# Kernel optimization log

Hardware: AMD Instinct MI355X
Metric: run time of the kernel (lower is better)

## Reference

```python
import jax, jax.numpy as jnp
import numpy as np
from jax import lax

# cell-group layout (order matters): sr_esoma, sr_edend, sr_pv, sr_sst, sr_vip, pfc_esoma, pfc_edend, pfc_pv, pfc_sst, pfc_vip
SIZES = [512, 1024, 128, 128, 128, 512, 1024, 128, 128, 128]
OFF = np.cumsum([0] + SIZES)
(SR_ES, SR_ED, SR_PV, SR_SST, SR_VIP,
 PFC_ES, PFC_ED, PFC_PV, PFC_SST, PFC_VIP) = [slice(int(OFF[i]), int(OFF[i + 1])) for i in range(10)]
N = int(OFF[-1])            # 3840 total neurons
N_BR = 2                    # dendritic branches per excitatory soma
N_IN, N_OUT = 128, 3
T, B = 100, 32
DT, TAU = 10.0, 50.0
DECAY = DT / TAU            # hp['dt']/hp['tau']
NOISE_STD = 0.01            # hp['network_noise']

# mGluR slow-integration coefficients on PFC E-dendrites: alpha_me = dt / logspace(100..5000), tiled over branches
_tau_me = np.tile(np.logspace(np.log10(100.0), np.log10(5000.0), SIZES[6] // N_BR), N_BR)
ALPHA_ME = jnp.asarray(DT / _tau_me, dtype=jnp.float32)   # [1024]

_dend = np.zeros(N, dtype=bool)
_dend[SR_ED] = True
_dend[PFC_ED] = True
DEND_VEC = jnp.asarray(_dend)


def _build_mask():
    """Dale's-law connectivity mask: +1 excitatory rows, -1 inhibitory rows,
    dend->own-region soma blocked (handled by dend2soma), zero diagonal."""
    m = np.ones((N, N), dtype=np.float32)
    for inh in (SR_PV, SR_SST, SR_VIP, PFC_PV, PFC_SST, PFC_VIP):
        m[inh, :] = -1.0
    m[SR_ED, SR_ES] = 0.0
    m[PFC_ED, PFC_ES] = 0.0
    np.fill_diagonal(m, 0.0)
    return m


def setup_inputs() -> dict:
    key = jax.random.key(0)
    ks = jax.random.split(key, 5)
    return {
        "x": jax.random.normal(ks[0], (T, B, N_IN), jnp.float32),
        "noise": jax.random.normal(ks[1], (T, B, N), jnp.float32),
        "w_rec": jax.random.normal(ks[2], (N, N), jnp.float32) / np.float32(np.sqrt(N)),
        "w_in": jax.random.normal(ks[3], (N_IN, N), jnp.float32) / np.float32(np.sqrt(N_IN)),
        "b": jnp.zeros((N,), jnp.float32),
        "d2s": jnp.ones((SIZES[1] + SIZES[6],), jnp.float32),
        "w_out": jax.random.normal(ks[4], (SIZES[0], N_OUT), jnp.float32) / np.float32(np.sqrt(SIZES[0])),
        "b_out": jnp.zeros((N_OUT,), jnp.float32),
        "mask": jnp.asarray(_build_mask()),
    }


def reference(x, noise, w_rec, w_in, b, d2s, w_out, b_out, mask):
    # effective recurrent weights: magnitude from w_rec, sign/sparsity from mask
    w_eff = jnp.abs(w_rec) * mask
    d2s_sr = d2s[:SIZES[1]].reshape(N_BR, SIZES[0])
    d2s_pfc = d2s[SIZES[1]:].reshape(N_BR, SIZES[5])
    nb = x.shape[1]
    h0 = jnp.zeros((nb, N), x.dtype)
    ime0 = jnp.zeros((nb, SIZES[6]), x.dtype)
    noise_scale = jnp.sqrt(jnp.asarray(2.0 * DECAY, x.dtype)) * NOISE_STD

    def step(carry, inp):
        h, ime = carry
        x_t, n_t = inp
        # rates: ReLU for somas/interneurons, sigmoidal dendritic nonlinearity for dendrites
        r = jnp.where(DEND_VEC[None, :], jax.nn.sigmoid(h), jax.nn.relu(h))
        pre = r @ w_eff + x_t @ w_in + b                      # [B, N]
        # dendrite -> soma coupling, summed over branches
        pre = pre.at[:, SR_ES].add(
            jnp.einsum('bkn,kn->bn', r[:, SR_ED].reshape(nb, N_BR, SIZES[0]), d2s_sr))
        pre = pre.at[:, PFC_ES].add(
            jnp.einsum('bkn,kn->bn', r[:, PFC_ED].reshape(nb, N_BR, SIZES[5]), d2s_pfc))
        # mGluR slow integration on PFC E-dendrites (per-dendrite time constants)
        ime_new = (1.0 - ALPHA_ME) * ime + ALPHA_ME * jax.nn.relu(pre[:, PFC_ED])
        pre = pre.at[:, PFC_ED].add(ime_new)
        # leaky integration with injected noise
        h_new = (1.0 - DECAY) * h + DECAY * pre + noise_scale * n_t
        out_t = r[:, SR_ES] @ w_out + b_out                   # readout from SR E somas
        return (h_new, ime_new), out_t

    _, outs = lax.scan(step, (h0, ime0), (x, noise))
    return outs   # [T, B, N_OUT]
```

## Files before the change

### kernel.cpp

```cpp
#include <hip/hip_runtime.h>
#include <math.h>

typedef _Float16 f16;
typedef f16 f16x8 __attribute__((ext_vector_type(8)));
typedef float f32x4 __attribute__((ext_vector_type(4)));

#define NTOT 3840
#define KP   3968
#define BATCH 32
#define TSTEPS 100
#define NIN 128
#define NWG 241
#define RSTRIDE (BATCH*KP)

__device__ __forceinline__ bool is_dend(int k){
  return (k>=512 && k<1536) || (k>=2432 && k<3456);
}
__device__ __forceinline__ bool is_inh(int k){
  return (k>=1536 && k<1920) || (k>=3456 && k<3840);
}
__device__ __forceinline__ ushort f2h(float v){ f16 h=(f16)v; return *(ushort*)&h; }
__device__ __forceinline__ float h2f(ushort u){ f16 h=*(f16*)&u; return (float)h; }

__global__ __launch_bounds__(256) void k_prep_w(const float* __restrict__ w_rec,
    const float* __restrict__ w_in, ushort* __restrict__ WT){
  __shared__ ushort tile[64][72];
  const int bid = blockIdx.x;
  const int kt = bid / 60, nt = bid % 60;
  const int k0 = kt*64, n0 = nt*64;
  const int t = threadIdx.x;
  const int tr = t>>2, tq = t&3;
  const int k = k0 + tr;
  const int cbase = n0 + tq*16;
  if (k < NTOT){
    const float sgn = is_inh(k) ? -1.f : 1.f;
    const bool rowSr  = (k>=512  && k<1536);
    const bool rowPfc = (k>=2432 && k<3456);
    #pragma unroll
    for (int q=0;q<4;q++){
      float4 w = *(const float4*)(w_rec + (size_t)k*NTOT + cbase + q*4);
      float v[4] = {sgn*fabsf(w.x), sgn*fabsf(w.y), sgn*fabsf(w.z), sgn*fabsf(w.w)};
      #pragma unroll
      for (int e=0;e<4;e++){
        const int n = cbase + q*4 + e;
        if (n==k || (rowSr && n<512) || (rowPfc && n>=1920 && n<2432)) v[e]=0.f;
        tile[tr][tq*16+q*4+e] = f2h(v[e]);
      }
    }
  } else {
    const float* src = w_in + (size_t)(k-NTOT)*NTOT + cbase;
    #pragma unroll
    for (int q=0;q<4;q++){
      float4 w = *(const float4*)(src + q*4);
      tile[tr][tq*16+q*4+0] = f2h(w.x);
      tile[tr][tq*16+q*4+1] = f2h(w.y);
      tile[tr][tq*16+q*4+2] = f2h(w.z);
      tile[tr][tq*16+q*4+3] = f2h(w.w);
    }
  }
  __syncthreads();
  const int n  = n0 + tr;
  const int kq = tq*16;
  uint u[8];
  #pragma unroll
  for (int q=0;q<8;q++)
    u[q] = (uint)tile[kq+2*q][tr] | ((uint)tile[kq+2*q+1][tr] << 16);
  uint4* dst = (uint4*)(WT + (size_t)n*KP + k0 + kq);
  dst[0] = make_uint4(u[0],u[1],u[2],u[3]);
  dst[1] = make_uint4(u[4],u[5],u[6],u[7]);
}

__global__ void k_init(const float* __restrict__ x, ushort* __restrict__ r0,
                       unsigned* __restrict__ bar){
  int i = blockIdx.x*blockDim.x + threadIdx.x;
  int nthr = gridDim.x*blockDim.x;
  for (int e=i; e<1024; e+=nthr) bar[e] = 0u;
  for (int e=i; e<BATCH*KP; e+=nthr){
    int b = e / KP, k = e % KP;
    float v = (k<NTOT) ? (is_dend(k)?0.5f:0.f) : x[b*NIN + (k-NTOT)];
    r0[e] = f2h(v);
  }
}

__global__ __launch_bounds__(512,1) void k_run(
    const ushort* __restrict__ WTu, ushort* rbase,
    const float* __restrict__ noise, const float* __restrict__ x,
    const float* __restrict__ bvec, const float* __restrict__ d2s,
    const float* __restrict__ w_out, const float* __restrict__ b_out,
    float* __restrict__ out, unsigned* bar)
{
  __shared__ ushort Blds[63488];
  __shared__ f32x4 red[3][2][64];
  __shared__ float pre_lds[32][16];
  const f16* WT = (const f16*)WTu;
  const int bid = blockIdx.x;
  const int tid = threadIdx.x;
  const int wv = tid>>6, l = tid&63, l15 = l&15, lh = l>>4;
  const int bh = wv&1, kw = wv>>1;
  const int n0 = bid*16;
  const int ub = tid>>4, uc = tid&15;
  const int n  = n0 + uc;
  const float NS = 0.0063245553203367585f;

  float hr=0.f, im=0.f, bv=0.f, dA=0.f, dB=0.f, al=0.f;
  bool cSR=false, cPFC=false, cME=false, dendF=false;
  if (bid < 240){
    bv = bvec[n];
    cSR  = (n0 < 512);
    cPFC = (n0 >= 1920 && n0 < 2432);
    cME  = (n0 >= 2432 && n0 < 3456);
    dendF = (n0>=512 && n0<1536) || cME;
    if (cSR){  dA=d2s[n];       dB=d2s[512+n]; }
    if (cPFC){ const int j=n-1920; dA=d2s[1024+j]; dB=d2s[1536+j]; }
    if (cME){
      const float LN10 = 2.302585092994046f;
      const float CEXP = 1.6989700043360187f/511.0f;
      const int j = n-2432;
      al = expf(-LN10*(1.0f + CEXP*(float)(j&511)));
    }
    for (int c = tid; c < 16*496; c += 512){
      const int row = c / 496;
      const int kc  = c - row*496;
      f16x8 v = *(const f16x8*)(WT + (size_t)(n0+row)*KP + kc*8);
      *(f16x8*)((char*)Blds + kc*256 + row*16) = v;
    }
  }

  float wo[3][8];
  float bo0=0.f, bo1=0.f, bo2=0.f;
  if (bid == 240){
    #pragma unroll
    for (int o=0;o<3;o++)
      #pragma unroll
      for (int i=0;i<8;i++) wo[o][i] = w_out[(l*8+i)*3 + o];
    bo0 = b_out[0]; bo1 = b_out[1]; bo2 = b_out[2];
  }
  __syncthreads();

  const int xg = bid & 7;
  const unsigned mycnt = (xg==0) ? 31u : 30u;
  unsigned* xcnt = bar + xg*32;
  unsigned* xep  = bar + 256 + xg*32;
  unsigned* gcnt = bar + 512;
  unsigned* gep  = bar + 544;

  const char* bb = (const char*)Blds + (kw*124 + lh)*256 + l15*16;

  for (int t=0; t<TSTEPS; t++){
    const ushort* rcu = rbase + (size_t)t*RSTRIDE;
    ushort*       rnu = rbase + (size_t)(t+1)*RSTRIDE;
    const f16* rc = (const f16*)rcu;

    if (bid < 240){
      const float nz_pf = noise[(size_t)t*BATCH*NTOT + ub*NTOT + n];
      float cA = 0.f, cB = 0.f;
      if (cSR){
        cA = h2f(rcu[ub*KP + 512 +n]); cB = h2f(rcu[ub*KP + 1024+n]);
      } else if (cPFC){
        const int j = n-1920;
        cA = h2f(rcu[ub*KP + 2432+j]); cB = h2f(rcu[ub*KP + 2944+j]);
      }

      f32x4 acc; acc.x=0.f; acc.y=0.f; acc.z=0.f; acc.w=0.f;
      {
        const f16* pa = rc + (size_t)(bh*16+l15)*KP + kw*992 + lh*8;
        #pragma unroll
        for (int ks=0; ks<31; ks++){
          f16x8 a = *(const f16x8*)(pa + ks*32);
          f16x8 b = *(const f16x8*)(bb + ks*1024);
          acc = __builtin_amdgcn_mfma_f32_16x16x32_f16(a, b, acc, 0,0,0);
        }
      }
      if (kw > 0) red[kw-1][bh][l] = acc;
      __syncthreads();
      if (kw == 0){
        #pragma unroll
        for (int w=0;w<3;w++) acc += red[w][bh][l];
        #pragma unroll
        for (int rg=0;rg<4;rg++)
          pre_lds[bh*16 + lh*4 + rg][l15] = acc[rg];
      }
      __syncthreads();

      {
        float p = pre_lds[ub][uc] + bv;
        p += cA*dA + cB*dB;
        if (cME){
          im = (1.f-al)*im + al*fmaxf(p,0.f); p += im;
        }
        hr = 0.8f*hr + 0.2f*p + NS*nz_pf;
        const float rv = dendF ? (1.f/(1.f+expf(-hr))) : fmaxf(hr,0.f);
        __hip_atomic_store(&rnu[ub*KP + n], f2h(rv),
                           __ATOMIC_RELAXED, __HIP_MEMORY_SCOPE_AGENT);
      }
    } else {
      #pragma unroll
      for (int q=0;q<12;q++){
        const int p = wv*12 + q;
        const int b = p/3, o = p%3;
        f16x8 rv8 = *(const f16x8*)(rc + (size_t)b*KP + l*8);
        float s = 0.f;
        #pragma unroll
        for (int i=0;i<8;i++) s += (float)rv8[i] * wo[o][i];
        #pragma unroll
        for (int off=32; off; off>>=1) s += __shfl_down(s, off);
        if (l==0){
          const float bo = (o==0)?bo0:((o==1)?bo1:bo2);
          out[t*BATCH*3 + b*3 + o] = s + bo;
        }
      }
      if (t+1 < TSTEPS && tid < 256){
        const int b = tid>>3, j = (tid&7)*16;
        const float* xs = x + (size_t)(t+1)*BATCH*NIN + b*NIN + j;
        #pragma unroll
        for (int q=0;q<4;q++){
          float4 v = *(const float4*)(xs + q*4);
          uint u0 = (uint)f2h(v.x) | ((uint)f2h(v.y)<<16);
          uint u1 = (uint)f2h(v.z) | ((uint)f2h(v.w)<<16);
          uint* dst = (uint*)&rnu[b*KP + NTOT + j + q*4];
          __hip_atomic_store(dst,   u0, __ATOMIC_RELAXED, __HIP_MEMORY_SCOPE_AGENT);
          __hip_atomic_store(dst+1, u1, __ATOMIC_RELAXED, __HIP_MEMORY_SCOPE_AGENT);
        }
      }
    }

    if (t+1 < TSTEPS){
      __syncthreads();
      if (tid == 0){
        unsigned old = __hip_atomic_fetch_add(xcnt, 1u,
                          __ATOMIC_RELAXED, __HIP_MEMORY_SCOPE_AGENT);
        if (old == mycnt*(unsigned)(t+1) - 1u){
          unsigned g = __hip_atomic_fetch_add(gcnt, 1u,
                          __ATOMIC_RELAXED, __HIP_MEMORY_SCOPE_AGENT);
          if (g == 8u*(unsigned)(t+1) - 1u){
            __hip_atomic_store(gep, (unsigned)(t+1),
                          __ATOMIC_RELAXED, __HIP_MEMORY_SCOPE_AGENT);
          } else {
            while (__hip_atomic_load(gep, __ATOMIC_RELAXED,
                          __HIP_MEMORY_SCOPE_AGENT) < (unsigned)(t+1))
              __builtin_amdgcn_s_sleep(2);
          }
          __hip_atomic_store(xep, (unsigned)(t+1),
                          __ATOMIC_RELAXED, __HIP_MEMORY_SCOPE_AGENT);
        } else {
          while (__hip_atomic_load(xep, __ATOMIC_RELAXED,
                          __HIP_MEMORY_SCOPE_AGENT) < (unsigned)(t+1))
            __builtin_amdgcn_s_sleep(2);
        }
        asm volatile("" ::: "memory");
      }
      __syncthreads();
    }
  }
}

extern "C" void kernel_launch(void* const* d_in, const int* in_sizes, int n_in,
                              void* d_out, int out_size, void* d_ws, size_t ws_size,
                              hipStream_t stream) {
  const float* x     = (const float*)d_in[0];
  const float* noise = (const float*)d_in[1];
  const float* w_rec = (const float*)d_in[2];
  const float* w_in  = (const float*)d_in[3];
  const float* bvec  = (const float*)d_in[4];
  const float* d2s   = (const float*)d_in[5];
  const float* w_out = (const float*)d_in[6];
  const float* b_out = (const float*)d_in[7];
  float* out = (float*)d_out;

  char* ws = (char*)d_ws;
  ushort*   WT    = (ushort*)(ws);
  ushort*   rbase = (ushort*)(ws + 30474240);
  unsigned* bar   = (unsigned*)(ws + 56123392);

  k_prep_w<<<3720,256,0,stream>>>(w_rec, w_in, WT);
  k_init<<<64,256,0,stream>>>(x, rbase, bar);
  k_run<<<NWG,512,0,stream>>>(WT, rbase, noise, x, bvec, d2s,
                              w_out, b_out, out, bar);
}
```

Before: 1.007 ms.

## Fuse epilogue into MFMA accumulator lanes and flatten hierarchical grid barrier

The per-neuron update (bias, dendrite coupling, mGluR integration, leak, nonlinearity, store) now runs directly on the wave-0 MFMA accumulator registers, four batch rows per lane. This removes the pre_lds scatter and one __syncthreads per step. The grid barrier is also reworked: the last arriving group leader writes all eight per-group epoch flags directly, and every block spins on its own group flag with a shorter sleep. This removes one level of release latency in the two-level barrier. The epilogue work is now concentrated in 128 threads instead of 512.

```diff
diff --git a/kernel.cpp b/kernel.cpp
--- a/kernel.cpp
+++ b/kernel.cpp
@@ -91,32 +91,35 @@
 {
   __shared__ ushort Blds[63488];
   __shared__ f32x4 red[3][2][64];
-  __shared__ float pre_lds[32][16];
   const f16* WT = (const f16*)WTu;
   const int bid = blockIdx.x;
   const int tid = threadIdx.x;
   const int wv = tid>>6, l = tid&63, l15 = l&15, lh = l>>4;
   const int bh = wv&1, kw = wv>>1;
   const int n0 = bid*16;
-  const int ub = tid>>4, uc = tid&15;
-  const int n  = n0 + uc;
+  const int n  = n0 + l15;
+  const int b0 = bh*16 + lh*4;
   const float NS = 0.0063245553203367585f;
 
-  float hr=0.f, im=0.f, bv=0.f, dA=0.f, dB=0.f, al=0.f;
+  float hr[4] = {0.f,0.f,0.f,0.f};
+  float im[4] = {0.f,0.f,0.f,0.f};
+  float bv=0.f, dA=0.f, dB=0.f, al=0.f;
   bool cSR=false, cPFC=false, cME=false, dendF=false;
   if (bid < 240){
-    bv = bvec[n];
-    cSR  = (n0 < 512);
-    cPFC = (n0 >= 1920 && n0 < 2432);
-    cME  = (n0 >= 2432 && n0 < 3456);
-    dendF = (n0>=512 && n0<1536) || cME;
-    if (cSR){  dA=d2s[n];       dB=d2s[512+n]; }
-    if (cPFC){ const int j=n-1920; dA=d2s[1024+j]; dB=d2s[1536+j]; }
-    if (cME){
-      const float LN10 = 2.302585092994046f;
-      const float CEXP = 1.6989700043360187f/511.0f;
-      const int j = n-2432;
-      al = expf(-LN10*(1.0f + CEXP*(float)(j&511)));
+    if (kw == 0){
+      bv = bvec[n];
+      cSR  = (n0 < 512);
+      cPFC = (n0 >= 1920 && n0 < 2432);
+      cME  = (n0 >= 2432 && n0 < 3456);
+      dendF = (n0>=512 && n0<1536) || cME;
+      if (cSR){  dA=d2s[n];       dB=d2s[512+n]; }
+      if (cPFC){ const int j=n-1920; dA=d2s[1024+j]; dB=d2s[1536+j]; }
+      if (cME){
+        const float LN10 = 2.302585092994046f;
+        const float CEXP = 1.6989700043360187f/511.0f;
+        const int j = n-2432;
+        al = expf(-LN10*(1.0f + CEXP*(float)(j&511)));
+      }
     }
     for (int c = tid; c < 16*496; c += 512){
       const int row = c / 496;
@@ -142,7 +145,6 @@
   unsigned* xcnt = bar + xg*32;
   unsigned* xep  = bar + 256 + xg*32;
   unsigned* gcnt = bar + 512;
-  unsigned* gep  = bar + 544;
 
   const char* bb = (const char*)Blds + (kw*124 + lh)*256 + l15*16;
 
@@ -152,13 +154,27 @@
     const f16* rc = (const f16*)rcu;
 
     if (bid < 240){
-      const float nz_pf = noise[(size_t)t*BATCH*NTOT + ub*NTOT + n];
-      float cA = 0.f, cB = 0.f;
-      if (cSR){
-        cA = h2f(rcu[ub*KP + 512 +n]); cB = h2f(rcu[ub*KP + 1024+n]);
-      } else if (cPFC){
-        const int j = n-1920;
-        cA = h2f(rcu[ub*KP + 2432+j]); cB = h2f(rcu[ub*KP + 2944+j]);
+      float nz[4] = {0.f,0.f,0.f,0.f};
+      float cA[4] = {0.f,0.f,0.f,0.f};
+      float cB[4] = {0.f,0.f,0.f,0.f};
+      if (kw == 0){
+        #pragma unroll
+        for (int rg=0;rg<4;rg++)
+          nz[rg] = noise[(size_t)t*BATCH*NTOT + (b0+rg)*NTOT + n];
+        if (cSR){
+          #pragma unroll
+          for (int rg=0;rg<4;rg++){
+            cA[rg] = h2f(rcu[(b0+rg)*KP + 512 +n]);
+            cB[rg] = h2f(rcu[(b0+rg)*KP + 1024+n]);
+          }
+        } else if (cPFC){
+          const int j = n-1920;
+          #pragma unroll
+          for (int rg=0;rg<4;rg++){
+            cA[rg] = h2f(rcu[(b0+rg)*KP + 2432+j]);
+            cB[rg] = h2f(rcu[(b0+rg)*KP + 2944+j]);
+          }
+        }
       }
 
       f32x4 acc; acc.x=0.f; acc.y=0.f; acc.z=0.f; acc.w=0.f;
@@ -177,21 +193,17 @@
         #pragma unroll
         for (int w=0;w<3;w++) acc += red[w][bh][l];
         #pragma unroll
-        for (int rg=0;rg<4;rg++)
-          pre_lds[bh*16 + lh*4 + rg][l15] = acc[rg];
-      }
-      __syncthreads();
-
-      {
-        float p = pre_lds[ub][uc] + bv;
-        p += cA*dA + cB*dB;
-        if (cME){
-          im = (1.f-al)*im + al*fmaxf(p,0.f); p += im;
-        }
-        hr = 0.8f*hr + 0.2f*p + NS*nz_pf;
-        const float rv = dendF ? (1.f/(1.f+expf(-hr))) : fmaxf(hr,0.f);
-        __hip_atomic_store(&rnu[ub*KP + n], f2h(rv),
-                           __ATOMIC_RELAXED, __HIP_MEMORY_SCOPE_AGENT);
+        for (int rg=0;rg<4;rg++){
+          float p = acc[rg] + bv;
+          p += cA[rg]*dA + cB[rg]*dB;
+          if (cME){
+            im[rg] = (1.f-al)*im[rg] + al*fmaxf(p,0.f); p += im[rg];
+          }
+          hr[rg] = 0.8f*hr[rg] + 0.2f*p + NS*nz[rg];
+          const float rv = dendF ? (1.f/(1.f+expf(-hr[rg]))) : fmaxf(hr[rg],0.f);
+          __hip_atomic_store(&rnu[(b0+rg)*KP + n], f2h(rv),
+                             __ATOMIC_RELAXED, __HIP_MEMORY_SCOPE_AGENT);
+        }
       }
     } else {
       #pragma unroll
@@ -233,20 +245,15 @@
           unsigned g = __hip_atomic_fetch_add(gcnt, 1u,
                           __ATOMIC_RELAXED, __HIP_MEMORY_SCOPE_AGENT);
           if (g == 8u*(unsigned)(t+1) - 1u){
-            __hip_atomic_store(gep, (unsigned)(t+1),
-                          __ATOMIC_RELAXED, __HIP_MEMORY_SCOPE_AGENT);
-          } else {
-            while (__hip_atomic_load(gep, __ATOMIC_RELAXED,
-                          __HIP_MEMORY_SCOPE_AGENT) < (unsigned)(t+1))
-              __builtin_amdgcn_s_sleep(2);
-          }
-          __hip_atomic_store(xep, (unsigned)(t+1),
-                          __ATOMIC_RELAXED, __HIP_MEMORY_SCOPE_AGENT);
-        } else {
-          while (__hip_atomic_load(xep, __ATOMIC_RELAXED,
-                          __HIP_MEMORY_SCOPE_AGENT) < (unsigned)(t+1))
-            __builtin_amdgcn_s_sleep(2);
-        }
+            #pragma unroll
+            for (int grp=0; grp<8; grp++)
+              __hip_atomic_store(bar + 256 + grp*32, (unsigned)(t+1),
+                            __ATOMIC_RELAXED, __HIP_MEMORY_SCOPE_AGENT);
+          }
+        }
+        while (__hip_atomic_load(xep, __ATOMIC_RELAXED,
+                      __HIP_MEMORY_SCOPE_AGENT) < (unsigned)(t+1))
+          __builtin_amdgcn_s_sleep(1);
         asm volatile("" ::: "memory");
       }
       __syncthreads();
```

Result: faster. 964.7 us (-4.2%).

## Drop second intra-block barrier and flatten grid barrier release

Applied to the files above, without the earlier changes.

The four k-split MFMA partials now all go to LDS, and each lane sums the element it owns directly. This removes the kw==0 reduction stage, the pre_lds staging buffer and one __syncthreads per step. The grid barrier also changes: the last group arriver writes all eight group epoch flags itself, so group leaders no longer spin on a global epoch and then re-publish it. Every block now polls its own group flag with a shorter sleep. The aim is to shorten the per-timestep critical path of the persistent kernel, at the cost of more serial flag stores and extra redundant LDS reads per lane.

```diff
diff --git a/kernel.cpp b/kernel.cpp
--- a/kernel.cpp
+++ b/kernel.cpp
@@ -90,19 +90,19 @@
     float* __restrict__ out, unsigned* bar)
 {
   __shared__ ushort Blds[63488];
-  __shared__ f32x4 red[3][2][64];
-  __shared__ float pre_lds[32][16];
+  __shared__ f32x4 red[4][2][64];
   const f16* WT = (const f16*)WTu;
   const int bid = blockIdx.x;
   const int tid = threadIdx.x;
   const int wv = tid>>6, l = tid&63, l15 = l&15, lh = l>>4;
   const int bh = wv&1, kw = wv>>1;
   const int n0 = bid*16;
-  const int ub = tid>>4, uc = tid&15;
-  const int n  = n0 + uc;
+  const int n  = n0 + l15;
+  const int br = bh*16 + lh*4 + kw;
   const float NS = 0.0063245553203367585f;
 
-  float hr=0.f, im=0.f, bv=0.f, dA=0.f, dB=0.f, al=0.f;
+  float hr = 0.f, im = 0.f;
+  float bv=0.f, dA=0.f, dB=0.f, al=0.f;
   bool cSR=false, cPFC=false, cME=false, dendF=false;
   if (bid < 240){
     bv = bvec[n];
@@ -142,7 +142,6 @@
   unsigned* xcnt = bar + xg*32;
   unsigned* xep  = bar + 256 + xg*32;
   unsigned* gcnt = bar + 512;
-  unsigned* gep  = bar + 544;
 
   const char* bb = (const char*)Blds + (kw*124 + lh)*256 + l15*16;
 
@@ -152,13 +151,13 @@
     const f16* rc = (const f16*)rcu;
 
     if (bid < 240){
-      const float nz_pf = noise[(size_t)t*BATCH*NTOT + ub*NTOT + n];
+      const float nz = noise[(size_t)t*BATCH*NTOT + br*NTOT + n];
       float cA = 0.f, cB = 0.f;
       if (cSR){
-        cA = h2f(rcu[ub*KP + 512 +n]); cB = h2f(rcu[ub*KP + 1024+n]);
+        cA = h2f(rcu[br*KP + 512 +n]); cB = h2f(rcu[br*KP + 1024+n]);
       } else if (cPFC){
         const int j = n-1920;
-        cA = h2f(rcu[ub*KP + 2432+j]); cB = h2f(rcu[ub*KP + 2944+j]);
+        cA = h2f(rcu[br*KP + 2432+j]); cB = h2f(rcu[br*KP + 2944+j]);
       }
 
       f32x4 acc; acc.x=0.f; acc.y=0.f; acc.z=0.f; acc.w=0.f;
@@ -171,26 +170,23 @@
           acc = __builtin_amdgcn_mfma_f32_16x16x32_f16(a, b, acc, 0,0,0);
         }
       }
-      if (kw > 0) red[kw-1][bh][l] = acc;
+      red[kw][bh][l] = acc;
       __syncthreads();
-      if (kw == 0){
-        #pragma unroll
-        for (int w=0;w<3;w++) acc += red[w][bh][l];
-        #pragma unroll
-        for (int rg=0;rg<4;rg++)
-          pre_lds[bh*16 + lh*4 + rg][l15] = acc[rg];
-      }
-      __syncthreads();
 
       {
-        float p = pre_lds[ub][uc] + bv;
+        float p = bv;
+        #pragma unroll
+        for (int w=0;w<4;w++){
+          f32x4 v = red[w][bh][l];
+          p += (kw==0) ? v.x : (kw==1) ? v.y : (kw==2) ? v.z : v.w;
+        }
         p += cA*dA + cB*dB;
         if (cME){
           im = (1.f-al)*im + al*fmaxf(p,0.f); p += im;
         }
-        hr = 0.8f*hr + 0.2f*p + NS*nz_pf;
+        hr = 0.8f*hr + 0.2f*p + NS*nz;
         const float rv = dendF ? (1.f/(1.f+expf(-hr))) : fmaxf(hr,0.f);
-        __hip_atomic_store(&rnu[ub*KP + n], f2h(rv),
+        __hip_atomic_store(&rnu[br*KP + n], f2h(rv),
                            __ATOMIC_RELAXED, __HIP_MEMORY_SCOPE_AGENT);
       }
     } else {
@@ -233,20 +229,15 @@
           unsigned g = __hip_atomic_fetch_add(gcnt, 1u,
                           __ATOMIC_RELAXED, __HIP_MEMORY_SCOPE_AGENT);
           if (g == 8u*(unsigned)(t+1) - 1u){
-            __hip_atomic_store(gep, (unsigned)(t+1),
-                          __ATOMIC_RELAXED, __HIP_MEMORY_SCOPE_AGENT);
-          } else {
-            while (__hip_atomic_load(gep, __ATOMIC_RELAXED,
-                          __HIP_MEMORY_SCOPE_AGENT) < (unsigned)(t+1))
-              __builtin_amdgcn_s_sleep(2);
+            #pragma unroll
+            for (int grp=0; grp<8; grp++)
+              __hip_atomic_store(bar + 256 + grp*32, (unsigned)(t+1),
+                            __ATOMIC_RELAXED, __HIP_MEMORY_SCOPE_AGENT);
           }
-          __hip_atomic_store(xep, (unsigned)(t+1),
-                          __ATOMIC_RELAXED, __HIP_MEMORY_SCOPE_AGENT);
-        } else {
-          while (__hip_atomic_load(xep, __ATOMIC_RELAXED,
-                          __HIP_MEMORY_SCOPE_AGENT) < (unsigned)(t+1))
-            __builtin_amdgcn_s_sleep(2);
-        }
+        }
+        while (__hip_atomic_load(xep, __ATOMIC_RELAXED,
+                      __HIP_MEMORY_SCOPE_AGENT) < (unsigned)(t+1))
+          __builtin_amdgcn_s_sleep(1);
         asm volatile("" ::: "memory");
       }
       __syncthreads();
```

Result: faster. 961.7 us (median of 3 runs) (-4.5%).
